# Optimization experiments

Hardware: AMD Instinct MI355X
Metric: run time of the kernel (lower is better)

## Reference

```python
import jax, jax.numpy as jnp
import numpy as np

TEMP = 0.05
EPS = 1e-12


def setup_inputs() -> dict:
    key = jax.random.key(0)
    k1, k2, k3, k4 = jax.random.split(key, 4)
    B, D, N = 2048, 128, 100000
    inputs = jax.random.normal(k1, (B, D), dtype=jnp.float32)
    indexes = jax.random.randint(k2, (B,), 0, N, dtype=jnp.int64)
    labels = jax.random.randint(k3, (N,), 0, N, dtype=jnp.int64)
    feats = jax.random.normal(k4, (N, D), dtype=jnp.float32)
    # memory bank rows are kept L2-normalized by the module's update logic
    features = feats / jnp.linalg.norm(feats, axis=1, keepdims=True)
    return {"inputs": inputs, "indexes": indexes, "labels": labels, "features": features}


def reference(inputs, indexes, labels, features):
    # F.normalize(inputs, dim=1)
    inputs_n = inputs / jnp.maximum(jnp.linalg.norm(inputs, axis=1, keepdims=True), EPS)
    # targets = labels[indexes]
    targets = labels[indexes]
    # logits = inputs_n @ features.T / temp  -> [B, N]
    logits = jnp.matmul(inputs_n, features.T) / TEMP
    # cross-entropy with mean reduction
    logz = jax.nn.logsumexp(logits, axis=1)
    picked = jnp.take_along_axis(logits, targets[:, None], axis=1)[:, 0]
    loss = jnp.mean(logz - picked)
    return loss
```

## Files before the change

kernel.cpp:

```cpp
#include <hip/hip_runtime.h>

typedef float f32x4 __attribute__((ext_vector_type(4)));
typedef int   int4v __attribute__((ext_vector_type(4)));
typedef int   int8v __attribute__((ext_vector_type(8)));

#define AS1 __attribute__((address_space(1)))
#define AS3 __attribute__((address_space(3)))

#define NROWS 2048
#define NCOLS 100000
#define NPAD  100352
#define NCHUNK 98
#define K2C  28.853900817779268f
#define PADC 7.2552607e-7f
#define SCLA 0x7F7F7F7Fu
#define SCLB 0x7C7C7C7Cu

__global__ void k_prep(const float* __restrict__ X, const int* __restrict__ idx,
                       const int* __restrict__ lab, const float* __restrict__ F,
                       unsigned short* __restrict__ A8, float* __restrict__ picked) {
  int wid = threadIdx.x >> 6, lane = threadIdx.x & 63;
  int row = blockIdx.x * 4 + wid;
  int t = lab[idx[row]];
  float2 v = ((const float2*)(X + (size_t)row * 128))[lane];
  float2 f = ((const float2*)(F + (size_t)t * 128))[lane];
  float ss = v.x * v.x + v.y * v.y;
  float dp = v.x * f.x + v.y * f.y;
#pragma unroll
  for (int m = 1; m < 64; m <<= 1) {
    ss += __shfl_xor(ss, m, 64);
    dp += __shfl_xor(dp, m, 64);
  }
  float invn = 1.0f / fmaxf(sqrtf(ss), 1e-12f);
  float s = invn * K2C;
  int w = __builtin_amdgcn_cvt_pk_fp8_f32(v.x * s, v.y * s, 0, false);
  A8[row * 64 + lane] = (unsigned short)(w & 0xFFFF);
  if (lane == 0) picked[row] = 20.0f * dp * invn;
}

__global__ void k_conv(const float* __restrict__ F, unsigned char* __restrict__ Fq) {
  const int NG16 = NPAD * 8;
  const int NV16 = NCOLS * 8;
  int stride = gridDim.x * blockDim.x;
  for (int g = blockIdx.x * blockDim.x + threadIdx.x; g < NG16; g += stride) {
    float4 a = make_float4(0.f, 0.f, 0.f, 0.f), b = a, c = a, d = a;
    if (g < NV16) {
      const float4* p = (const float4*)F + 4 * (size_t)g;
      a = p[0]; b = p[1]; c = p[2]; d = p[3];
    }
    int w0 = __builtin_amdgcn_cvt_pk_fp8_f32(a.x * 8.f, a.y * 8.f, 0, false);
    w0 = __builtin_amdgcn_cvt_pk_fp8_f32(a.z * 8.f, a.w * 8.f, w0, true);
    int w1 = __builtin_amdgcn_cvt_pk_fp8_f32(b.x * 8.f, b.y * 8.f, 0, false);
    w1 = __builtin_amdgcn_cvt_pk_fp8_f32(b.z * 8.f, b.w * 8.f, w1, true);
    int w2 = __builtin_amdgcn_cvt_pk_fp8_f32(c.x * 8.f, c.y * 8.f, 0, false);
    w2 = __builtin_amdgcn_cvt_pk_fp8_f32(c.z * 8.f, c.w * 8.f, w2, true);
    int w3 = __builtin_amdgcn_cvt_pk_fp8_f32(d.x * 8.f, d.y * 8.f, 0, false);
    w3 = __builtin_amdgcn_cvt_pk_fp8_f32(d.z * 8.f, d.w * 8.f, w3, true);
    ((int4v*)Fq)[g] = (int4v){w0, w1, w2, w3};
  }
}

__global__ __launch_bounds__(256, 2) void k_gemm(
    const unsigned short* __restrict__ A8,
    const unsigned char* __restrict__ Fq,
    float* __restrict__ part) {
  __shared__ unsigned char ring[3][64 * 128];
  __shared__ float xpose[4][64];
  const int tid = threadIdx.x;
  const int wid = tid >> 6, lane = tid & 63;
  const int lrow = lane & 15, lk = lane >> 4;

  const int slot = blockIdx.x >> 3;
  const int xcd  = blockIdx.x & 7;
  const int mtile = slot & 7;
  const int chunk = (slot >> 3) * 8 + xcd;
  if (chunk >= NCHUNK) return;
  const int row0 = mtile * 256 + wid * 64;

  const unsigned char* A8b = (const unsigned char*)A8;
  int8v af[4];
#pragma unroll
  for (int mf = 0; mf < 4; ++mf) {
    const unsigned char* ap = A8b + (size_t)(row0 + mf * 16 + lrow) * 128 + lk * 32;
    ((int4v*)&af[mf])[0] = *(const int4v*)ap;
    ((int4v*)&af[mf])[1] = *(const int4v*)(ap + 16);
  }

  f32x4 racc[4];
#pragma unroll
  for (int mf = 0; mf < 4; ++mf) racc[mf] = (f32x4){0.f, 0.f, 0.f, 0.f};

  f32x4 cinit = (f32x4){-K2C, -K2C, -K2C, -K2C};

  int dsoff[4][2];
#pragma unroll
  for (int j = 0; j < 4; ++j) {
    int c = j * 16 + lrow, x = c & 7;
    dsoff[j][0] = c * 128 + (((lk * 2)     ^ x) * 16);
    dsoff[j][1] = c * 128 + (((lk * 2 + 1) ^ x) * 16);
  }

  const int nbase = chunk * 1024;

  auto issue1 = [&](unsigned char* dst, int h, int it) {
    int off16 = it * 256 + tid;
    int col = off16 >> 3, up = off16 & 7;
    int ul = up ^ (col & 7);
    const unsigned char* src = Fq + (size_t)(nbase + h * 64 + col) * 128 + ul * 16;
    __builtin_amdgcn_global_load_lds((const AS1 void*)src,
                                     (AS3 void*)(dst + off16 * 16), 16, 0, 0);
  };

  auto half_body = [&](const unsigned char* sb, unsigned char* stDst, int hst) {
#pragma unroll
    for (int j = 0; j < 4; ++j) {
      int8v b8;
      ((int4v*)&b8)[0] = *(const int4v*)(sb + dsoff[j][0]);
      ((int4v*)&b8)[1] = *(const int4v*)(sb + dsoff[j][1]);
      if (stDst && (j & 1) == 0) issue1(stDst, hst, j >> 1);
      f32x4 acc[4];
#pragma unroll
      for (int mf = 0; mf < 4; ++mf)
        acc[mf] = __builtin_amdgcn_mfma_scale_f32_16x16x128_f8f6f4(
            af[mf], b8, cinit, 0, 0, 0, SCLA, 0, SCLB);
#pragma unroll
      for (int mf = 0; mf < 4; ++mf) {
        f32x4 e;
        e[0] = __builtin_amdgcn_exp2f(acc[mf][0]);
        e[1] = __builtin_amdgcn_exp2f(acc[mf][1]);
        e[2] = __builtin_amdgcn_exp2f(acc[mf][2]);
        e[3] = __builtin_amdgcn_exp2f(acc[mf][3]);
        racc[mf] += e;
      }
    }
  };

#pragma unroll
  for (int h = 0; h < 2; ++h)
#pragma unroll
    for (int it = 0; it < 2; ++it) issue1(&ring[h][0], h, it);

  int rs = 0;
#pragma unroll 1
  for (int h = 0; h < 14; ++h) {
    asm volatile("s_waitcnt vmcnt(2)" ::: "memory");
    __builtin_amdgcn_s_barrier();
    int ss = rs + 2 - (rs >= 1 ? 3 : 0);
    half_body(&ring[rs][0], &ring[ss][0], h + 2);
    rs = (rs == 2) ? 0 : rs + 1;
  }
  asm volatile("s_waitcnt vmcnt(2)" ::: "memory");
  __builtin_amdgcn_s_barrier();
  half_body(&ring[rs][0], nullptr, 0);
  rs = (rs == 2) ? 0 : rs + 1;
  asm volatile("s_waitcnt vmcnt(0)" ::: "memory");
  __builtin_amdgcn_s_barrier();
  half_body(&ring[rs][0], nullptr, 0);

#pragma unroll
  for (int mf = 0; mf < 4; ++mf)
#pragma unroll
    for (int j = 0; j < 4; ++j) {
      float v = racc[mf][j];
      v += __shfl_xor(v, 1, 64);
      v += __shfl_xor(v, 2, 64);
      v += __shfl_xor(v, 4, 64);
      v += __shfl_xor(v, 8, 64);
      if (lrow == 0) xpose[wid][mf * 16 + lk * 4 + j] = v;
    }
  __syncthreads();
  part[(size_t)chunk * NROWS + row0 + lane] = xpose[wid][lane];
}

__global__ void k_loss1(const float* __restrict__ part, float* __restrict__ psum) {
  int rb = blockIdx.x & 7, cb = blockIdx.x >> 3;
  int b = rb * 256 + threadIdx.x;
  float s = 0.f;
#pragma unroll
  for (int k = 0; k < 14; ++k)
    s += part[(size_t)(cb * 14 + k) * NROWS + b];
  psum[(size_t)cb * NROWS + b] = s;
}

__global__ void k_final(const float* __restrict__ psum, const float* __restrict__ picked,
                        float* __restrict__ out) {
  int tid = threadIdx.x;
  float lb = 0.f;
#pragma unroll
  for (int rr = 0; rr < 2; ++rr) {
    int b = rr * 1024 + tid;
    float tot = 0.f;
#pragma unroll
    for (int cb = 0; cb < 7; ++cb) tot += psum[(size_t)cb * NROWS + b];
    tot -= PADC;
    lb += 20.0f + logf(tot) - picked[b];
  }
#pragma unroll
  for (int m = 1; m < 64; m <<= 1) lb += __shfl_xor(lb, m, 64);
  __shared__ float red[16];
  if ((tid & 63) == 0) red[tid >> 6] = lb;
  __syncthreads();
  if (tid == 0) {
    float s = 0.f;
#pragma unroll
    for (int i = 0; i < 16; ++i) s += red[i];
    out[0] = s * (1.0f / 2048.0f);
  }
}

extern "C" void kernel_launch(void* const* d_in, const int* in_sizes, int n_in,
                              void* d_out, int out_size, void* d_ws, size_t ws_size,
                              hipStream_t stream) {
  const float* inputs  = (const float*)d_in[0];
  const int*   indexes = (const int*)d_in[1];
  const int*   labels  = (const int*)d_in[2];
  const float* feats   = (const float*)d_in[3];
  float* out = (float*)d_out;

  char* ws = (char*)d_ws;
  unsigned short* A8 = (unsigned short*)(ws + 0);
  unsigned char*  Fq = (unsigned char*)(ws + 262144);
  float* part   = (float*)(ws + 13107200);
  float* psum   = (float*)(ws + 13910016);
  float* picked = (float*)(ws + 13967360);

  hipLaunchKernelGGL(k_prep,  dim3(512),  dim3(256),  0, stream, inputs, indexes, labels, feats, A8, picked);
  hipLaunchKernelGGL(k_conv,  dim3(1568), dim3(256),  0, stream, feats, Fq);
  hipLaunchKernelGGL(k_gemm,  dim3(832),  dim3(256),  0, stream, A8, Fq, part);
  hipLaunchKernelGGL(k_loss1, dim3(56),   dim3(256),  0, stream, part, psum);
  hipLaunchKernelGGL(k_final, dim3(1),    dim3(1024), 0, stream, psum, picked, out);
}
```

Measured before the change: 65.75 us.

## Merge prep and conversion kernels; restructure GEMM pipeline into paired double-buffered stages

The input-normalisation and feature-bank fp8 conversion kernels are merged into one launch, with the block index choosing the role, which removes one kernel launch and its gap. The GEMM main loop now processes two 64-column sub-tiles per barrier using a 4-slot LDS ring as a double buffer of pairs. This halves the number of barriers and interleaves twice as many independent MFMAs between exp2 work. In exchange it waits with vmcnt(0) each step, so prefetch depth relative to compute is reduced, and LDS use grows, which may affect the two-blocks-per-CU occupancy.

```diff
diff --git a/kernel.cpp b/kernel.cpp
--- a/kernel.cpp
+++ b/kernel.cpp
@@ -16,47 +16,48 @@
 #define SCLA 0x7F7F7F7Fu
 #define SCLB 0x7C7C7C7Cu
 
-__global__ void k_prep(const float* __restrict__ X, const int* __restrict__ idx,
-                       const int* __restrict__ lab, const float* __restrict__ F,
-                       unsigned short* __restrict__ A8, float* __restrict__ picked) {
-  int wid = threadIdx.x >> 6, lane = threadIdx.x & 63;
-  int row = blockIdx.x * 4 + wid;
-  int t = lab[idx[row]];
-  float2 v = ((const float2*)(X + (size_t)row * 128))[lane];
-  float2 f = ((const float2*)(F + (size_t)t * 128))[lane];
-  float ss = v.x * v.x + v.y * v.y;
-  float dp = v.x * f.x + v.y * f.y;
-#pragma unroll
-  for (int m = 1; m < 64; m <<= 1) {
-    ss += __shfl_xor(ss, m, 64);
-    dp += __shfl_xor(dp, m, 64);
-  }
-  float invn = 1.0f / fmaxf(sqrtf(ss), 1e-12f);
-  float s = invn * K2C;
-  int w = __builtin_amdgcn_cvt_pk_fp8_f32(v.x * s, v.y * s, 0, false);
-  A8[row * 64 + lane] = (unsigned short)(w & 0xFFFF);
-  if (lane == 0) picked[row] = 20.0f * dp * invn;
-}
-
-__global__ void k_conv(const float* __restrict__ F, unsigned char* __restrict__ Fq) {
-  const int NG16 = NPAD * 8;
-  const int NV16 = NCOLS * 8;
-  int stride = gridDim.x * blockDim.x;
-  for (int g = blockIdx.x * blockDim.x + threadIdx.x; g < NG16; g += stride) {
-    float4 a = make_float4(0.f, 0.f, 0.f, 0.f), b = a, c = a, d = a;
-    if (g < NV16) {
-      const float4* p = (const float4*)F + 4 * (size_t)g;
-      a = p[0]; b = p[1]; c = p[2]; d = p[3];
-    }
-    int w0 = __builtin_amdgcn_cvt_pk_fp8_f32(a.x * 8.f, a.y * 8.f, 0, false);
-    w0 = __builtin_amdgcn_cvt_pk_fp8_f32(a.z * 8.f, a.w * 8.f, w0, true);
-    int w1 = __builtin_amdgcn_cvt_pk_fp8_f32(b.x * 8.f, b.y * 8.f, 0, false);
-    w1 = __builtin_amdgcn_cvt_pk_fp8_f32(b.z * 8.f, b.w * 8.f, w1, true);
-    int w2 = __builtin_amdgcn_cvt_pk_fp8_f32(c.x * 8.f, c.y * 8.f, 0, false);
-    w2 = __builtin_amdgcn_cvt_pk_fp8_f32(c.z * 8.f, c.w * 8.f, w2, true);
-    int w3 = __builtin_amdgcn_cvt_pk_fp8_f32(d.x * 8.f, d.y * 8.f, 0, false);
-    w3 = __builtin_amdgcn_cvt_pk_fp8_f32(d.z * 8.f, d.w * 8.f, w3, true);
-    ((int4v*)Fq)[g] = (int4v){w0, w1, w2, w3};
+__global__ void k_pc(const float* __restrict__ X, const int* __restrict__ idx,
+                     const int* __restrict__ lab, const float* __restrict__ F,
+                     unsigned short* __restrict__ A8, float* __restrict__ picked,
+                     unsigned char* __restrict__ Fq) {
+  if (blockIdx.x < 512) {
+    int wid = threadIdx.x >> 6, lane = threadIdx.x & 63;
+    int row = blockIdx.x * 4 + wid;
+    int t = lab[idx[row]];
+    float2 v = ((const float2*)(X + (size_t)row * 128))[lane];
+    float2 f = ((const float2*)(F + (size_t)t * 128))[lane];
+    float ss = v.x * v.x + v.y * v.y;
+    float dp = v.x * f.x + v.y * f.y;
+#pragma unroll
+    for (int m = 1; m < 64; m <<= 1) {
+      ss += __shfl_xor(ss, m, 64);
+      dp += __shfl_xor(dp, m, 64);
+    }
+    float invn = 1.0f / fmaxf(sqrtf(ss), 1e-12f);
+    float s = invn * K2C;
+    int w = __builtin_amdgcn_cvt_pk_fp8_f32(v.x * s, v.y * s, 0, false);
+    A8[row * 64 + lane] = (unsigned short)(w & 0xFFFF);
+    if (lane == 0) picked[row] = 20.0f * dp * invn;
+  } else {
+    const int NG16 = NPAD * 8;
+    const int NV16 = NCOLS * 8;
+    int stride = 1568 * 256;
+    for (int g = (blockIdx.x - 512) * 256 + threadIdx.x; g < NG16; g += stride) {
+      float4 a = make_float4(0.f, 0.f, 0.f, 0.f), b = a, c = a, d = a;
+      if (g < NV16) {
+        const float4* p = (const float4*)F + 4 * (size_t)g;
+        a = p[0]; b = p[1]; c = p[2]; d = p[3];
+      }
+      int w0 = __builtin_amdgcn_cvt_pk_fp8_f32(a.x * 8.f, a.y * 8.f, 0, false);
+      w0 = __builtin_amdgcn_cvt_pk_fp8_f32(a.z * 8.f, a.w * 8.f, w0, true);
+      int w1 = __builtin_amdgcn_cvt_pk_fp8_f32(b.x * 8.f, b.y * 8.f, 0, false);
+      w1 = __builtin_amdgcn_cvt_pk_fp8_f32(b.z * 8.f, b.w * 8.f, w1, true);
+      int w2 = __builtin_amdgcn_cvt_pk_fp8_f32(c.x * 8.f, c.y * 8.f, 0, false);
+      w2 = __builtin_amdgcn_cvt_pk_fp8_f32(c.z * 8.f, c.w * 8.f, w2, true);
+      int w3 = __builtin_amdgcn_cvt_pk_fp8_f32(d.x * 8.f, d.y * 8.f, 0, false);
+      w3 = __builtin_amdgcn_cvt_pk_fp8_f32(d.z * 8.f, d.w * 8.f, w3, true);
+      ((int4v*)Fq)[g] = (int4v){w0, w1, w2, w3};
+    }
   }
 }
 
@@ -64,7 +65,7 @@
     const unsigned short* __restrict__ A8,
     const unsigned char* __restrict__ Fq,
     float* __restrict__ part) {
-  __shared__ unsigned char ring[3][64 * 128];
+  __shared__ unsigned char ring[4][64 * 128];
   __shared__ float xpose[4][64];
   const int tid = threadIdx.x;
   const int wid = tid >> 6, lane = tid & 63;
@@ -111,51 +112,60 @@
                                      (AS3 void*)(dst + off16 * 16), 16, 0, 0);
   };
 
-  auto half_body = [&](const unsigned char* sb, unsigned char* stDst, int hst) {
+  auto pair_body = [&](const unsigned char* sbA, const unsigned char* sbB,
+                       bool doStage, int nslot, int hnext) {
 #pragma unroll
     for (int j = 0; j < 4; ++j) {
-      int8v b8;
-      ((int4v*)&b8)[0] = *(const int4v*)(sb + dsoff[j][0]);
-      ((int4v*)&b8)[1] = *(const int4v*)(sb + dsoff[j][1]);
-      if (stDst && (j & 1) == 0) issue1(stDst, hst, j >> 1);
-      f32x4 acc[4];
+      int8v b8A, b8B;
+      ((int4v*)&b8A)[0] = *(const int4v*)(sbA + dsoff[j][0]);
+      ((int4v*)&b8A)[1] = *(const int4v*)(sbA + dsoff[j][1]);
+      ((int4v*)&b8B)[0] = *(const int4v*)(sbB + dsoff[j][0]);
+      ((int4v*)&b8B)[1] = *(const int4v*)(sbB + dsoff[j][1]);
+      if (doStage)
+        issue1(&ring[nslot + (j >> 1)][0], hnext + (j >> 1), j & 1);
+      f32x4 accA[4], accB[4];
 #pragma unroll
       for (int mf = 0; mf < 4; ++mf)
-        acc[mf] = __builtin_amdgcn_mfma_scale_f32_16x16x128_f8f6f4(
-            af[mf], b8, cinit, 0, 0, 0, SCLA, 0, SCLB);
+        accA[mf] = __builtin_amdgcn_mfma_scale_f32_16x16x128_f8f6f4(
+            af[mf], b8A, cinit, 0, 0, 0, SCLA, 0, SCLB);
+#pragma unroll
+      for (int mf = 0; mf < 4; ++mf)
+        accB[mf] = __builtin_amdgcn_mfma_scale_f32_16x16x128_f8f6f4(
+            af[mf], b8B, cinit, 0, 0, 0, SCLA, 0, SCLB);
 #pragma unroll
       for (int mf = 0; mf < 4; ++mf) {
         f32x4 e;
-        e[0] = __builtin_amdgcn_exp2f(acc[mf][0]);
-        e[1] = __builtin_amdgcn_exp2f(acc[mf][1]);
-        e[2] = __builtin_amdgcn_exp2f(acc[mf][2]);
-        e[3] = __builtin_amdgcn_exp2f(acc[mf][3]);
+        e[0] = __builtin_amdgcn_exp2f(accA[mf][0]);
+        e[1] = __builtin_amdgcn_exp2f(accA[mf][1]);
+        e[2] = __builtin_amdgcn_exp2f(accA[mf][2]);
+        e[3] = __builtin_amdgcn_exp2f(accA[mf][3]);
         racc[mf] += e;
       }
+#pragma unroll
+      for (int mf = 0; mf < 4; ++mf) {
+        f32x4 e;
+        e[0] = __builtin_amdgcn_exp2f(accB[mf][0]);
+        e[1] = __builtin_amdgcn_exp2f(accB[mf][1]);
+        e[2] = __builtin_amdgcn_exp2f(accB[mf][2]);
+        e[3] = __builtin_amdgcn_exp2f(accB[mf][3]);
+        racc[mf] += e;
+      }
     }
   };
 
-#pragma unroll
-  for (int h = 0; h < 2; ++h)
-#pragma unroll
-    for (int it = 0; it < 2; ++it) issue1(&ring[h][0], h, it);
-
-  int rs = 0;
+  issue1(&ring[0][0], 0, 0);
+  issue1(&ring[0][0], 0, 1);
+  issue1(&ring[1][0], 1, 0);
+  issue1(&ring[1][0], 1, 1);
+
 #pragma unroll 1
-  for (int h = 0; h < 14; ++h) {
-    asm volatile("s_waitcnt vmcnt(2)" ::: "memory");
+  for (int i = 0; i < 8; ++i) {
+    asm volatile("s_waitcnt vmcnt(0)" ::: "memory");
     __builtin_amdgcn_s_barrier();
-    int ss = rs + 2 - (rs >= 1 ? 3 : 0);
-    half_body(&ring[rs][0], &ring[ss][0], h + 2);
-    rs = (rs == 2) ? 0 : rs + 1;
-  }
-  asm volatile("s_waitcnt vmcnt(2)" ::: "memory");
-  __builtin_amdgcn_s_barrier();
-  half_body(&ring[rs][0], nullptr, 0);
-  rs = (rs == 2) ? 0 : rs + 1;
-  asm volatile("s_waitcnt vmcnt(0)" ::: "memory");
-  __builtin_amdgcn_s_barrier();
-  half_body(&ring[rs][0], nullptr, 0);
+    int s0 = (i & 1) * 2;
+    int n0 = 2 - s0;
+    pair_body(&ring[s0][0], &ring[s0 + 1][0], i < 7, n0, 2 * i + 2);
+  }
 
 #pragma unroll
   for (int mf = 0; mf < 4; ++mf)
@@ -224,8 +234,7 @@
   float* psum   = (float*)(ws + 13910016);
   float* picked = (float*)(ws + 13967360);
 
-  hipLaunchKernelGGL(k_prep,  dim3(512),  dim3(256),  0, stream, inputs, indexes, labels, feats, A8, picked);
-  hipLaunchKernelGGL(k_conv,  dim3(1568), dim3(256),  0, stream, feats, Fq);
+  hipLaunchKernelGGL(k_pc,    dim3(2080), dim3(256),  0, stream, inputs, indexes, labels, feats, A8, picked, Fq);
   hipLaunchKernelGGL(k_gemm,  dim3(832),  dim3(256),  0, stream, A8, Fq, part);
   hipLaunchKernelGGL(k_loss1, dim3(56),   dim3(256),  0, stream, part, psum);
   hipLaunchKernelGGL(k_final, dim3(1),    dim3(1024), 0, stream, psum, picked, out);
```

Result: faster. 62.35 us, median of 2 (-5.2%).
